# Performance work log

Hardware: AMD Instinct MI355X
Metric: run time of the kernel (lower is better)

Reference implementation:

```python
import math
import jax, jax.numpy as jnp
import numpy as np

C = 1024
H = 16
HD = C // H
T = 2048
B = 2
EPS = 1e-5


def setup_inputs() -> dict:
    key = jax.random.key(0)
    ks = jax.random.split(key, 8)
    s = 0.02
    return {
        "x": jax.random.normal(ks[0], (B, T, C), dtype=jnp.float32),
        "ln1_g": jnp.ones((C,), jnp.float32),
        "ln1_b": jnp.zeros((C,), jnp.float32),
        "w_attn": jax.random.normal(ks[1], (C, 3 * C), dtype=jnp.float32) * s,
        "b_attn": jnp.zeros((3 * C,), jnp.float32),
        "w_proj": jax.random.normal(ks[2], (C, C), dtype=jnp.float32) * s,
        "b_proj": jnp.zeros((C,), jnp.float32),
        "ln2_g": jnp.ones((C,), jnp.float32),
        "ln2_b": jnp.zeros((C,), jnp.float32),
        "w_fc": jax.random.normal(ks[3], (C, 4 * C), dtype=jnp.float32) * s,
        "b_fc": jnp.zeros((4 * C,), jnp.float32),
        "w_fc2": jax.random.normal(ks[4], (4 * C, C), dtype=jnp.float32) * s,
        "b_fc2": jnp.zeros((C,), jnp.float32),
    }


def _layernorm(x, g, b):
    mu = jnp.mean(x, axis=-1, keepdims=True)
    var = jnp.mean((x - mu) ** 2, axis=-1, keepdims=True)
    return (x - mu) * jax.lax.rsqrt(var + EPS) * g + b


def _attention(x, w_attn, b_attn, w_proj, b_proj):
    Bb, Tt, Cc = x.shape
    qkv = x @ w_attn + b_attn  # (B,T,3C)
    q, k, v = jnp.split(qkv, 3, axis=-1)
    # (B,H,T,HD)
    q = q.reshape(Bb, Tt, H, HD).transpose(0, 2, 1, 3)
    k = k.reshape(Bb, Tt, H, HD).transpose(0, 2, 1, 3)
    v = v.reshape(Bb, Tt, H, HD).transpose(0, 2, 1, 3)
    scale = 1.0 / math.sqrt(HD)
    attn = jnp.einsum("bhqd,bhkd->bhqk", q, k) * scale
    causal = jnp.tril(jnp.ones((Tt, Tt), dtype=bool))
    attn = jnp.where(causal[None, None], attn, -jnp.inf)
    attn = jax.nn.softmax(attn, axis=-1)
    out = jnp.einsum("bhqk,bhkd->bhqd", attn, v)
    out = out.transpose(0, 2, 1, 3).reshape(Bb, Tt, Cc)
    return out @ w_proj + b_proj


def _mlp(x, w_fc, b_fc, w_fc2, b_fc2):
    h = jax.nn.gelu(x @ w_fc + b_fc, approximate=True)
    return h @ w_fc2 + b_fc2


def reference(x, ln1_g, ln1_b, w_attn, b_attn, w_proj, b_proj,
              ln2_g, ln2_b, w_fc, b_fc, w_fc2, b_fc2):
    x = x + _attention(_layernorm(x, ln1_g, ln1_b), w_attn, b_attn, w_proj, b_proj)
    x = x + _mlp(_layernorm(x, ln2_g, ln2_b), w_fc, b_fc, w_fc2, b_fc2)
    return x
```

## Files before the change

### kernel.cpp

```cpp
#include <hip/hip_runtime.h>
#include <math.h>

#define TB 2
#define TT 2048
#define TC 1024
#define TH 16
#define THD 64
#define TM (TB*TT)
#define NQT 32

typedef __bf16 bf16x8 __attribute__((ext_vector_type(8)));
typedef float f32x4 __attribute__((ext_vector_type(4)));
typedef unsigned short u16x8 __attribute__((ext_vector_type(8)));
typedef unsigned short u16x4 __attribute__((ext_vector_type(4)));

__device__ __forceinline__ unsigned short f2bf(float f){
    unsigned int u = __builtin_bit_cast(unsigned int, f);
    u = (u + 0x7FFFu + ((u >> 16) & 1u)) >> 16;
    return (unsigned short)u;
}
__device__ __forceinline__ float bf2f(unsigned short h){
    unsigned int u = ((unsigned int)h) << 16;
    return __builtin_bit_cast(float, u);
}
__device__ __forceinline__ bf16x8 ldbf8(const unsigned short* p){
    return __builtin_bit_cast(bf16x8, *(const u16x8*)p);
}
__device__ __forceinline__ void gl_lds16(const void* g, void* l){
    __builtin_amdgcn_global_load_lds(
        (const __attribute__((address_space(1))) unsigned int*)g,
        (__attribute__((address_space(3))) unsigned int*)l,
        16, 0, 0);
}
__device__ __forceinline__ float gelu_tanh(float v){
    float u = 2.0f * 0.7978845608028654f * (v + 0.044715f * v * v * v);
    u = fminf(fmaxf(u, -30.f), 30.f);
    float e = __expf(u);
    return 0.5f * v * (1.f + (e - 1.f) / (e + 1.f));
}

__global__ __launch_bounds__(256)
void prep_all(const float* __restrict__ w_attn, const float* __restrict__ w_proj,
              const float* __restrict__ w_fc,   const float* __restrict__ w_fc2,
              unsigned short* __restrict__ wattnT, unsigned short* __restrict__ wprojT,
              unsigned short* __restrict__ wfcT,   unsigned short* __restrict__ wfc2T,
              const float* __restrict__ x, const float* __restrict__ ln1_g,
              const float* __restrict__ ln1_b, unsigned short* __restrict__ xn1){
    const int bid = blockIdx.x;
    const int t = threadIdx.x;
    if (bid >= 12288){
        const int row = bid - 12288;
        const float4* xr = (const float4*)(x + (size_t)row * TC);
        float4 v = xr[t];
        float s  = v.x + v.y + v.z + v.w;
        float s2 = v.x*v.x + v.y*v.y + v.z*v.z + v.w*v.w;
        #pragma unroll
        for (int off = 32; off; off >>= 1){
            s  += __shfl_down(s,  off);
            s2 += __shfl_down(s2, off);
        }
        __shared__ float red[8];
        int l = t & 63, wv = t >> 6;
        if (l == 0){ red[wv] = s; red[4 + wv] = s2; }
        __syncthreads();
        float S  = red[0] + red[1] + red[2] + red[3];
        float S2 = red[4] + red[5] + red[6] + red[7];
        float mu = S * (1.f / TC);
        float var = S2 * (1.f / TC) - mu * mu;
        float rs = rsqrtf(var + 1e-5f);
        int c = t * 4;
        float4 gg = *(const float4*)(ln1_g + c);
        float4 bb = *(const float4*)(ln1_b + c);
        u16x4 o;
        o[0] = f2bf((v.x - mu) * rs * gg.x + bb.x);
        o[1] = f2bf((v.y - mu) * rs * gg.y + bb.y);
        o[2] = f2bf((v.z - mu) * rs * gg.z + bb.z);
        o[3] = f2bf((v.w - mu) * rs * gg.w + bb.w);
        *(u16x4*)(xn1 + (size_t)row * TC + c) = o;
        return;
    }
    __shared__ float tile[32][33];
    const float* in; unsigned short* out; int K, N, bx, by;
    if (bid < 3072)      { in=w_attn; out=wattnT; K=1024; N=3072; bx=bid%96;  by=bid/96; }
    else if (bid < 4096) { int lo=bid-3072; in=w_proj; out=wprojT; K=1024; N=1024; bx=lo%32;  by=lo/32; }
    else if (bid < 8192) { int lo=bid-4096; in=w_fc;   out=wfcT;   K=1024; N=4096; bx=lo%128; by=lo/128; }
    else                 { int lo=bid-8192; in=w_fc2;  out=wfc2T;  K=4096; N=1024; bx=lo%32;  by=lo/32; }
    int tx = t & 31, ty = t >> 5;
    int n0 = bx * 32, k0 = by * 32;
    #pragma unroll
    for (int i = 0; i < 4; i++)
        tile[ty + 8*i][tx] = in[(size_t)(k0 + ty + 8*i) * N + n0 + tx];
    __syncthreads();
    #pragma unroll
    for (int i = 0; i < 4; i++)
        out[(size_t)(n0 + ty + 8*i) * K + k0 + tx] = f2bf(tile[tx][ty + 8*i]);
}

__global__ __launch_bounds__(256)
void ln_kernel(const float* __restrict__ x, const float* __restrict__ g,
               const float* __restrict__ be, unsigned short* __restrict__ y){
    const int row = blockIdx.x, t = threadIdx.x;
    const float4* xr = (const float4*)(x + (size_t)row * TC);
    float4 v = xr[t];
    float s  = v.x + v.y + v.z + v.w;
    float s2 = v.x*v.x + v.y*v.y + v.z*v.z + v.w*v.w;
    #pragma unroll
    for (int off = 32; off; off >>= 1){
        s  += __shfl_down(s,  off);
        s2 += __shfl_down(s2, off);
    }
    __shared__ float red[8];
    int l = t & 63, wv = t >> 6;
    if (l == 0){ red[wv] = s; red[4 + wv] = s2; }
    __syncthreads();
    float S  = red[0] + red[1] + red[2] + red[3];
    float S2 = red[4] + red[5] + red[6] + red[7];
    float mu = S * (1.f / TC);
    float var = S2 * (1.f / TC) - mu * mu;
    float rs = rsqrtf(var + 1e-5f);
    int c = t * 4;
    float4 gg = *(const float4*)(g + c);
    float4 bb = *(const float4*)(be + c);
    u16x4 o;
    o[0] = f2bf((v.x - mu) * rs * gg.x + bb.x);
    o[1] = f2bf((v.y - mu) * rs * gg.y + bb.y);
    o[2] = f2bf((v.z - mu) * rs * gg.z + bb.z);
    o[3] = f2bf((v.w - mu) * rs * gg.w + bb.w);
    *(u16x4*)(y + (size_t)row * TC + c) = o;
}

template<int EPI>
__global__ __launch_bounds__(256, 2)
void gemm_bt(const unsigned short* __restrict__ A,
             const unsigned short* __restrict__ Bt,
             const float* __restrict__ bias,
             const float* __restrict__ resid,
             void* __restrict__ outv,
             int M, int N, int K){
    __shared__ unsigned short lA[128 * 32];
    __shared__ unsigned short lB[128 * 32];
    const int t = threadIdx.x, w = t >> 6, l = t & 63, lr = l & 15, lg = l >> 4;
    const int nt = N >> 7;
    const int nwg = gridDim.x;
    const int bid = blockIdx.x;
    int wg = (nwg & 7) ? bid : ((bid & 7) * (nwg >> 3) + (bid >> 3));
    const int bm = wg / nt, bn = wg % nt;
    const int row0 = bm << 7, col0 = bn << 7;
    const int wr = w >> 1, wc = w & 1;

    f32x4 acc[4][4];
    #pragma unroll
    for (int i = 0; i < 4; i++)
        #pragma unroll
        for (int j = 0; j < 4; j++) acc[i][j] = (f32x4){0.f,0.f,0.f,0.f};

    const char* Ag = (const char*)(A + (size_t)(row0 + (t >> 2)) * K) + (t & 3) * 16;
    const char* Bg = (const char*)(Bt + (size_t)(col0 + (t >> 2)) * K) + (t & 3) * 16;
    const size_t rstep = (size_t)64 * K * 2;
    char* lAw = (char*)lA + w * 1024;
    char* lBw = (char*)lB + w * 1024;

    for (int k0 = 0; k0 < K; k0 += 32){
        size_t kb = (size_t)k0 * 2;
        gl_lds16(Ag + kb,          lAw);
        gl_lds16(Ag + kb + rstep,  lAw + 4096);
        gl_lds16(Bg + kb,          lBw);
        gl_lds16(Bg + kb + rstep,  lBw + 4096);
        __syncthreads();
        bf16x8 af[4], bfr[4];
        #pragma unroll
        for (int mi = 0; mi < 4; mi++)
            af[mi] = ldbf8(lA + (wr*64 + mi*16 + lr) * 32 + lg * 8);
        #pragma unroll
        for (int ni = 0; ni < 4; ni++)
            bfr[ni] = ldbf8(lB + (wc*64 + ni*16 + lr) * 32 + lg * 8);
        #pragma unroll
        for (int mi = 0; mi < 4; mi++)
            #pragma unroll
            for (int ni = 0; ni < 4; ni++)
                acc[mi][ni] = __builtin_amdgcn_mfma_f32_16x16x32_bf16(
                    af[mi], bfr[ni], acc[mi][ni], 0, 0, 0);
        __syncthreads();
    }

    float bcol[4];
    #pragma unroll
    for (int ni = 0; ni < 4; ni++) bcol[ni] = bias[col0 + wc*64 + ni*16 + lr];
    #pragma unroll
    for (int mi = 0; mi < 4; mi++){
        #pragma unroll
        for (int j = 0; j < 4; j++){
            int row = row0 + wr*64 + mi*16 + lg*4 + j;
            size_t base = (size_t)row * N + col0 + wc*64 + lr;
            #pragma unroll
            for (int ni = 0; ni < 4; ni++){
                float v = acc[mi][ni][j] + bcol[ni];
                size_t idx = base + (size_t)ni * 16;
                if (EPI == 0)      ((unsigned short*)outv)[idx] =
                    __builtin_bit_cast(unsigned short, (__bf16)v);
                else if (EPI == 1) ((float*)outv)[idx] = v + resid[idx];
                else               ((unsigned short*)outv)[idx] =
                    __builtin_bit_cast(unsigned short, (__bf16)gelu_tanh(v));
            }
        }
    }
}

template<int MH>
__device__ __forceinline__ void gloadA(const unsigned short* bufA, bf16x8 (&af)[4][2],
                                       int wm, int lr, int sl0, int sl1){
    #pragma unroll
    for (int i = 0; i < 4; i++){
        int lrow = (wm*128 + (MH*4 + i)*16 + lr) * 64;
        af[i][0] = ldbf8(bufA + lrow + sl0);
        af[i][1] = ldbf8(bufA + lrow + sl1);
    }
}
__device__ __forceinline__ void gloadB(const unsigned short* bufB, bf16x8 (&bfr)[4][2],
                                       int wn, int lr, int sl0, int sl1){
    #pragma unroll
    for (int i = 0; i < 4; i++){
        int brow = (wn*64 + i*16 + lr) * 64;
        bfr[i][0] = ldbf8(bufB + brow + sl0);
        bfr[i][1] = ldbf8(bufB + brow + sl1);
    }
}
template<int MH, int NH>
__device__ __forceinline__ void gmma(const bf16x8 (&af)[4][2], const bf16x8 (&bfr)[4][2],
                                     f32x4 (&acc)[8][4]){
    #pragma unroll
    for (int i = 0; i < 4; i++)
        #pragma unroll
        for (int j = 0; j < 2; j++){
            f32x4& a = acc[MH*4 + i][NH*2 + j];
            a = __builtin_amdgcn_mfma_f32_16x16x32_bf16(af[i][0], bfr[NH*2+j][0], a, 0,0,0);
            a = __builtin_amdgcn_mfma_f32_16x16x32_bf16(af[i][1], bfr[NH*2+j][1], a, 0,0,0);
        }
}

#define G256_LOOP(NT_, KBEG_)                                                   \
    for (int tk = 0; tk < (NT_); ++tk){                                         \
        const int cur = tk & 1;                                                 \
        const bool more1 = (tk + 1) < (NT_);                                    \
        const bool more2 = (tk + 2) < (NT_);                                    \
        const unsigned short* bufA = &lds[cur][0][0];                           \
        const unsigned short* bufB = &lds[cur][1][0];                           \
        if (more1) asm volatile("s_waitcnt vmcnt(2)" ::: "memory");             \
        else       asm volatile("s_waitcnt vmcnt(0)" ::: "memory");             \
        __builtin_amdgcn_s_barrier();                                           \
        {                                                                       \
            bf16x8 afr[4][2], bfr[4][2];                                        \
            gloadA<0>(bufA, afr, wm, lr, sl0, sl1);                             \
            gloadB(bufB, bfr, wn, lr, sl0, sl1);                                \
            if (more1){                                                         \
                stage(cur ^ 1, (KBEG_) + (tk + 1)*64, 1);                       \
                stage(cur ^ 1, (KBEG_) + (tk + 1)*64, 2);                       \
            }                                                                   \
            __builtin_amdgcn_s_setprio(1);                                      \
            gmma<0,0>(afr, bfr, acc);                                           \
            gmma<0,1>(afr, bfr, acc);                                           \
            __builtin_amdgcn_s_setprio(0);                                      \
            gloadA<1>(bufA, afr, wm, lr, sl0, sl1);                             \
            if (more1) stage(cur ^ 1, (KBEG_) + (tk + 1)*64, 3);                \
            __builtin_amdgcn_s_setprio(1);                                      \
            gmma<1,0>(afr, bfr, acc);                                           \
            gmma<1,1>(afr, bfr, acc);                                           \
            __builtin_amdgcn_s_setprio(0);                                      \
        }                                                                       \
        __builtin_amdgcn_s_barrier();                                           \
        if (more2) stage(cur, (KBEG_) + (tk + 2)*64, 0);                        \
    }

template<int EPI>
__global__ __launch_bounds__(512, 1)
void gemm256(const unsigned short* __restrict__ A,
             const unsigned short* __restrict__ Bt,
             const float* __restrict__ bias,
             void* __restrict__ outv,
             int M, int N, int K){
    __shared__ unsigned short lds[2][2][256*64];
    const int t = threadIdx.x;
    const int w = t >> 6, l = t & 63, lr = l & 15, lg = l >> 4;
    const int wm = w >> 2, wn = w & 3;
    const int lr7 = lr & 7;
    const int sl0 = (lg ^ lr7) << 3;
    const int sl1 = ((4 + lg) ^ lr7) << 3;
    const int nbn = N >> 8;
    const int nwg = (M >> 8) * nbn;
    const int bid = blockIdx.x;
    const int wg = (nwg & 7) ? bid : ((bid & 7) * (nwg >> 3) + (bid >> 3));
    const int bm = wg / nbn, bn = wg % nbn;
    const size_t row0 = (size_t)bm << 8, col0 = (size_t)bn << 8;
    const int NT = K >> 6;

    f32x4 acc[8][4];
    #pragma unroll
    for (int i = 0; i < 8; i++)
        #pragma unroll
        for (int j = 0; j < 4; j++) acc[i][j] = (f32x4){0.f,0.f,0.f,0.f};

    int rowc[4], slogc[4];
    #pragma unroll
    for (int c = 0; c < 4; c++){
        int seg = t + (c << 9);
        rowc[c]  = seg >> 3;
        slogc[c] = (((seg & 7) ^ ((seg >> 3) & 7)) << 3);
    }
    const unsigned short* Abase = A  + row0 * K;
    const unsigned short* Bbase = Bt + col0 * K;
    auto stage = [&](int buf, int kofs, int c){
        int seg = t + (c << 9);
        const unsigned short* sa = Abase + (size_t)rowc[c] * K + kofs + slogc[c];
        const unsigned short* sb = Bbase + (size_t)rowc[c] * K + kofs + slogc[c];
        gl_lds16(sa, (void*)&lds[buf][0][seg * 8]);
        gl_lds16(sb, (void*)&lds[buf][1][seg * 8]);
    };

    #pragma unroll
    for (int c = 0; c < 4; c++) stage(0, 0, c);
    if (NT > 1) stage(1, 64, 0);

    G256_LOOP(NT, 0)

    float bcol[4];
    #pragma unroll
    for (int ni = 0; ni < 4; ni++) bcol[ni] = bias[col0 + wn*64 + ni*16 + lr];
    unsigned short* outp = (unsigned short*)outv;
    #pragma unroll
    for (int mi = 0; mi < 8; mi++){
        #pragma unroll
        for (int j = 0; j < 4; j++){
            size_t row = row0 + wm*128 + mi*16 + lg*4 + j;
            size_t base = row * N + col0 + wn*64 + lr;
            #pragma unroll
            for (int ni = 0; ni < 4; ni++){
                float v = acc[mi][ni][j] + bcol[ni];
                size_t idx = base + (size_t)ni * 16;
                if (EPI == 0) outp[idx] = __builtin_bit_cast(unsigned short, (__bf16)v);
                else          outp[idx] = __builtin_bit_cast(unsigned short, (__bf16)gelu_tanh(v));
            }
        }
    }
}

__global__ __launch_bounds__(512, 1)
void gemm256sk(const unsigned short* __restrict__ A,
               const unsigned short* __restrict__ Bt,
               unsigned short* __restrict__ pout,
               int M, int N, int K, int klen){
    __shared__ unsigned short lds[2][2][256*64];
    const int t = threadIdx.x;
    const int w = t >> 6, l = t & 63, lr = l & 15, lg = l >> 4;
    const int wm = w >> 2, wn = w & 3;
    const int lr7 = lr & 7;
    const int sl0 = (lg ^ lr7) << 3;
    const int sl1 = ((4 + lg) ^ lr7) << 3;
    const int nbn = N >> 8;
    const int ntile = (M >> 8) * nbn;
    const int nwg = gridDim.x;
    const int bid = blockIdx.x;
    int wg = (nwg & 7) ? bid : ((bid & 7) * (nwg >> 3) + (bid >> 3));
    const int kh = wg / ntile;
    wg -= kh * ntile;
    const int bm = wg / nbn, bn = wg % nbn;
    const size_t row0 = (size_t)bm << 8, col0 = (size_t)bn << 8;
    const int NT = klen >> 6;
    const int kbeg = kh * klen;

    f32x4 acc[8][4];
    #pragma unroll
    for (int i = 0; i < 8; i++)
        #pragma unroll
        for (int j = 0; j < 4; j++) acc[i][j] = (f32x4){0.f,0.f,0.f,0.f};

    int rowc[4], slogc[4];
    #pragma unroll
    for (int c = 0; c < 4; c++){
        int seg = t + (c << 9);
        rowc[c]  = seg >> 3;
        slogc[c] = (((seg & 7) ^ ((seg >> 3) & 7)) << 3);
    }
    const unsigned short* Abase = A  + row0 * K;
    const unsigned short* Bbase = Bt + col0 * K;
    auto stage = [&](int buf, int kofs, int c){
        int seg = t + (c << 9);
        const unsigned short* sa = Abase + (size_t)rowc[c] * K + kofs + slogc[c];
        const unsigned short* sb = Bbase + (size_t)rowc[c] * K + kofs + slogc[c];
        gl_lds16(sa, (void*)&lds[buf][0][seg * 8]);
        gl_lds16(sb, (void*)&lds[buf][1][seg * 8]);
    };

    #pragma unroll
    for (int c = 0; c < 4; c++) stage(0, kbeg, c);
    if (NT > 1) stage(1, kbeg + 64, 0);

    G256_LOOP(NT, kbeg)

    unsigned short* outp = pout + (size_t)kh * M * N;
    #pragma unroll
    for (int mi = 0; mi < 8; mi++){
        #pragma unroll
        for (int j = 0; j < 4; j++){
            size_t row = row0 + wm*128 + mi*16 + lg*4 + j;
            size_t base = row * N + col0 + wn*64 + lr;
            #pragma unroll
            for (int ni = 0; ni < 4; ni++)
                outp[base + (size_t)ni * 16] =
                    __builtin_bit_cast(unsigned short, (__bf16)acc[mi][ni][j]);
        }
    }
}

__global__ __launch_bounds__(256)
void combine_k4(const unsigned short* __restrict__ p,
                const float* __restrict__ bias, const float* __restrict__ resid,
                float* __restrict__ out){
    const size_t PS = (size_t)TM * TC;
    const int total = TM * TC / 4;
    for (int i = blockIdx.x * 256 + threadIdx.x; i < total; i += gridDim.x * 256){
        int e = i * 4;
        u16x4 a0 = *(const u16x4*)(p + e);
        u16x4 a1 = *(const u16x4*)(p + PS + e);
        u16x4 a2 = *(const u16x4*)(p + 2*PS + e);
        u16x4 a3 = *(const u16x4*)(p + 3*PS + e);
        float4 r = *(const float4*)(resid + e);
        float4 bb = *(const float4*)(bias + (e & (TC - 1)));
        float4 o;
        o.x = bf2f(a0[0]) + bf2f(a1[0]) + bf2f(a2[0]) + bf2f(a3[0]) + r.x + bb.x;
        o.y = bf2f(a0[1]) + bf2f(a1[1]) + bf2f(a2[1]) + bf2f(a3[1]) + r.y + bb.y;
        o.z = bf2f(a0[2]) + bf2f(a1[2]) + bf2f(a2[2]) + bf2f(a3[2]) + r.z + bb.z;
        o.w = bf2f(a0[3]) + bf2f(a1[3]) + bf2f(a2[3]) + bf2f(a3[3]) + r.w + bb.w;
        *(float4*)(out + e) = o;
    }
}

__global__ __launch_bounds__(256)
void vtrans(const unsigned short* __restrict__ qkv, unsigned short* __restrict__ vTg){
    __shared__ unsigned short lt[64][68];
    int kt = blockIdx.x & (NQT - 1);
    int bh = blockIdx.x >> 5;
    int h = bh & (TH - 1), b = bh >> 4;
    int t = threadIdx.x;
    int r = t >> 2, c4 = t & 3;
    const unsigned short* src = qkv + (size_t)(b*TT + kt*64 + r) * (3*TC) + 2*TC + h*THD;
    u16x8 a0 = *(const u16x8*)(src + c4*8);
    u16x8 a1 = *(const u16x8*)(src + 32 + c4*8);
    #pragma unroll
    for (int j = 0; j < 8; j++){
        lt[r][c4*8 + j]      = a0[j];
        lt[r][32 + c4*8 + j] = a1[j];
    }
    __syncthreads();
    int d = t >> 2;
    unsigned short* dst = vTg + ((size_t)bh * NQT + kt) * (64*80) + (size_t)d * 80;
    u16x8 o0, o1;
    #pragma unroll
    for (int j = 0; j < 8; j++){
        o0[j] = lt[c4*8 + j][d];
        o1[j] = lt[32 + c4*8 + j][d];
    }
    *(u16x8*)(dst + c4*8)      = o0;
    *(u16x8*)(dst + 32 + c4*8) = o1;
}

__global__ __launch_bounds__(256, 3)
void attn_kernel(const unsigned short* __restrict__ qkv,
                 const unsigned short* __restrict__ vTg,
                 unsigned short* __restrict__ attn_out){
    __shared__ unsigned short kbuf[128*64];
    __shared__ unsigned short vbuf[128*64];
    __shared__ unsigned short pl[4][16*136];

    const int bid = blockIdx.x;
    const int qrank = bid >> 5;
    const int bh = bid & 31;
    const int h = bh & (TH - 1), b = bh >> 4;
    const int qb = 31 - qrank;
    const int q0 = qb << 6;
    const int t = threadIdx.x, w = t >> 6, l = t & 63, lr = l & 15, lg = l >> 4;
    const int lr7 = lr & 7;
    const int sl0 = (lg ^ lr7) << 3;
    const int sl1 = ((4 + lg) ^ lr7) << 3;
    const float SC = 0.18033688011112042f;

    const int NP = (qb >> 1) + 1;
    const int qrow_base = q0 + w*16;
    const int myq = qrow_base + lr;

    const unsigned short* kgp[4];
    const unsigned short* vgp[4];
    #pragma unroll
    for (int p = 0; p < 4; p++){
        int vt = p*256 + t;
        int r  = vt >> 3;
        int sc = ((vt & 7) ^ (r & 7)) * 8;
        kgp[p] = qkv + (size_t)(b*TT + r) * (3*TC) + TC + h*THD + sc;
        vgp[p] = vTg + (size_t)bh * (NQT*64*80)
               + (size_t)(r >> 6) * (64*80) + (size_t)(r & 63) * 80 + sc;
    }
    const size_t kstep2 = (size_t)128 * (3*TC);
    const size_t vstep2 = (size_t)2 * (64*80);

    auto stage_k = [&](int pi){
        #pragma unroll
        for (int p = 0; p < 4; p++)
            gl_lds16(kgp[p] + (size_t)pi*kstep2, (void*)&kbuf[(p*256 + t)*8]);
    };
    auto stage_v = [&](int pi){
        #pragma unroll
        for (int p = 0; p < 4; p++)
            gl_lds16(vgp[p] + (size_t)pi*vstep2, (void*)&vbuf[(p*256 + t)*8]);
    };

    const unsigned short* qr =
        qkv + (size_t)(b*TT + myq) * (3*TC) + h*THD;
    bf16x8 q0f = ldbf8(qr + lg*8), q1f = ldbf8(qr + 32 + lg*8);

    bf16x8 ones;
    #pragma unroll
    for (int i = 0; i < 8; i++) ones[i] = (__bf16)1.0f;

    f32x4 o[5];
    float m = -1e30f;
    #pragma unroll
    for (int i = 0; i < 5; i++) o[i] = (f32x4){0.f,0.f,0.f,0.f};

    unsigned short* plw = &pl[w][0];

    stage_k(0);
    for (int pi = 0; pi < NP; ++pi){
        const int t0 = 2*pi, t1 = 2*pi + 1;
        asm volatile("s_waitcnt vmcnt(0)" ::: "memory");
        __builtin_amdgcn_s_barrier();
        stage_v(pi);

        f32x4 s[8];
        __builtin_amdgcn_s_setprio(1);
        #pragma unroll
        for (int cb = 0; cb < 8; cb++){
            bf16x8 ka = ldbf8(kbuf + (cb*16 + lr)*64 + sl0);
            bf16x8 kbf = ldbf8(kbuf + (cb*16 + lr)*64 + sl1);
            f32x4 z = (f32x4){0.f,0.f,0.f,0.f};
            z = __builtin_amdgcn_mfma_f32_16x16x32_bf16(ka, q0f, z, 0,0,0);
            z = __builtin_amdgcn_mfma_f32_16x16x32_bf16(kbf, q1f, z, 0,0,0);
            s[cb] = z;
        }
        __builtin_amdgcn_s_setprio(0);
        if (t0 == qb){
            #pragma unroll
            for (int cb = 0; cb < 4; cb++)
                #pragma unroll
                for (int j = 0; j < 4; j++)
                    if (t0*64 + cb*16 + lg*4 + j > myq) s[cb][j] = -1e30f;
        }
        if (t1 == qb){
            #pragma unroll
            for (int cb = 4; cb < 8; cb++)
                #pragma unroll
                for (int j = 0; j < 4; j++)
                    if (t1*64 + (cb-4)*16 + lg*4 + j > myq) s[cb][j] = -1e30f;
        } else if (t1 > qb){
            #pragma unroll
            for (int cb = 4; cb < 8; cb++)
                #pragma unroll
                for (int j = 0; j < 4; j++) s[cb][j] = -1e30f;
        }
        float mloc = s[0][0];
        #pragma unroll
        for (int cb = 0; cb < 8; cb++)
            #pragma unroll
            for (int j = 0; j < 4; j++) mloc = fmaxf(mloc, s[cb][j]);
        mloc = fmaxf(mloc, __shfl_xor(mloc, 16));
        mloc = fmaxf(mloc, __shfl_xor(mloc, 32));
        bool grow = (mloc * SC > m);
        float al = 1.f;
        if (__any(grow)){
            float mn = fmaxf(m, mloc * SC);
            al = exp2f(m - mn);
            m = mn;
            float alb[4];
            #pragma unroll
            for (int j = 0; j < 4; j++) alb[j] = __shfl(al, lg*4 + j);
            #pragma unroll
            for (int db = 0; db < 5; db++)
                #pragma unroll
                for (int j = 0; j < 4; j++) o[db][j] *= alb[j];
        }
        #pragma unroll
        for (int cb = 0; cb < 8; cb++){
            u16x4 pk;
            #pragma unroll
            for (int j = 0; j < 4; j++){
                float e = exp2f(__builtin_fmaf(s[cb][j], SC, -m));
                pk[j] = __builtin_bit_cast(unsigned short, (__bf16)e);
            }
            *(u16x4*)(plw + lr*136 + cb*16 + lg*4) = pk;
        }
        asm volatile("s_waitcnt vmcnt(0)" ::: "memory");
        __builtin_amdgcn_s_barrier();
        if (pi + 1 < NP) stage_k(pi + 1);

        bf16x8 pa0 = ldbf8(plw + lr*136 + lg*8);
        bf16x8 pa1 = ldbf8(plw + lr*136 + 32 + lg*8);
        bf16x8 pa2 = ldbf8(plw + lr*136 + 64 + lg*8);
        bf16x8 pa3 = ldbf8(plw + lr*136 + 96 + lg*8);
        __builtin_amdgcn_s_setprio(1);
        #pragma unroll
        for (int db = 0; db < 4; db++){
            bf16x8 v0a = ldbf8(vbuf + (db*16 + lr)*64 + sl0);
            bf16x8 v0b = ldbf8(vbuf + (db*16 + lr)*64 + sl1);
            o[db] = __builtin_amdgcn_mfma_f32_16x16x32_bf16(pa0, v0a, o[db], 0,0,0);
            o[db] = __builtin_amdgcn_mfma_f32_16x16x32_bf16(pa1, v0b, o[db], 0,0,0);
            bf16x8 v1a = ldbf8(vbuf + (64 + db*16 + lr)*64 + sl0);
            bf16x8 v1b = ldbf8(vbuf + (64 + db*16 + lr)*64 + sl1);
            o[db] = __builtin_amdgcn_mfma_f32_16x16x32_bf16(pa2, v1a, o[db], 0,0,0);
            o[db] = __builtin_amdgcn_mfma_f32_16x16x32_bf16(pa3, v1b, o[db], 0,0,0);
        }
        o[4] = __builtin_amdgcn_mfma_f32_16x16x32_bf16(pa0, ones, o[4], 0,0,0);
        o[4] = __builtin_amdgcn_mfma_f32_16x16x32_bf16(pa1, ones, o[4], 0,0,0);
        o[4] = __builtin_amdgcn_mfma_f32_16x16x32_bf16(pa2, ones, o[4], 0,0,0);
        o[4] = __builtin_amdgcn_mfma_f32_16x16x32_bf16(pa3, ones, o[4], 0,0,0);
        __builtin_amdgcn_s_setprio(0);
    }

    __bf16* aout = (__bf16*)attn_out;
    #pragma unroll
    for (int j = 0; j < 4; j++){
        float inv = 1.f / o[4][j];
        size_t tok = (size_t)(b*TT + qrow_base + lg*4 + j);
        #pragma unroll
        for (int db = 0; db < 4; db++)
            aout[tok*TC + h*THD + db*16 + lr] = (__bf16)(o[db][j] * inv);
    }
}

extern "C" void kernel_launch(void* const* d_in, const int* in_sizes, int n_in,
                              void* d_out, int out_size, void* d_ws, size_t ws_size,
                              hipStream_t stream){
    const float* x      = (const float*)d_in[0];
    const float* ln1_g  = (const float*)d_in[1];
    const float* ln1_b  = (const float*)d_in[2];
    const float* w_attn = (const float*)d_in[3];
    const float* b_attn = (const float*)d_in[4];
    const float* w_proj = (const float*)d_in[5];
    const float* b_proj = (const float*)d_in[6];
    const float* ln2_g  = (const float*)d_in[7];
    const float* ln2_b  = (const float*)d_in[8];
    const float* w_fc   = (const float*)d_in[9];
    const float* b_fc   = (const float*)d_in[10];
    const float* w_fc2  = (const float*)d_in[11];
    const float* b_fc2  = (const float*)d_in[12];
    float* out = (float*)d_out;

    char* ws = (char*)d_ws;
    size_t off = 0;
    auto alloc = [&](size_t bytes) -> void* {
        void* p = ws + off;
        off += (bytes + 255) & ~(size_t)255;
        return p;
    };
    unsigned short* wattnT = (unsigned short*)alloc((size_t)3072*1024*2);
    unsigned short* wprojT = (unsigned short*)alloc((size_t)1024*1024*2);
    unsigned short* wfcT   = (unsigned short*)alloc((size_t)4096*1024*2);
    unsigned short* wfc2T  = (unsigned short*)alloc((size_t)1024*4096*2);
    unsigned short* xn1    = (unsigned short*)alloc((size_t)TM*TC*2);
    unsigned short* qkvb   = (unsigned short*)alloc((size_t)TM*3*TC*2);
    float*          resid1 = (float*)alloc((size_t)TM*TC*4);
    unsigned short* xn2    = (unsigned short*)alloc((size_t)TM*TC*2);
    unsigned short* hbuf   = (unsigned short*)alloc((size_t)TM*4*TC*2);
    unsigned short* attnO  = (unsigned short*)alloc((size_t)TM*TC*2);
    unsigned short* vTg    = (unsigned short*)alloc((size_t)TB*TH*NQT*64*80*2);

    unsigned short* pks = xn1;

    prep_all<<<12288 + TM, 256, 0, stream>>>(
        w_attn, w_proj, w_fc, w_fc2, wattnT, wprojT, wfcT, wfc2T,
        x, ln1_g, ln1_b, xn1);

    gemm256<0><<<(TM/256)*(3072/256), 512, 0, stream>>>(
        xn1, wattnT, b_attn, qkvb, TM, 3072, 1024);

    vtrans<<<TB*TH*NQT, 256, 0, stream>>>(qkvb, vTg);

    attn_kernel<<<TB*TH*NQT, 256, 0, stream>>>(qkvb, vTg, attnO);

    gemm_bt<1><<<(TM/128)*(1024/128), 256, 0, stream>>>(
        attnO, wprojT, b_proj, x, resid1, TM, 1024, 1024);

    ln_kernel<<<TM, 256, 0, stream>>>(resid1, ln2_g, ln2_b, xn2);

    gemm256<2><<<(TM/256)*(4096/256), 512, 0, stream>>>(
        xn2, wfcT, b_fc, hbuf, TM, 4096, 1024);

    gemm256sk<<<4*(TM/256)*(1024/256), 512, 0, stream>>>(
        hbuf, wfc2T, pks, TM, 1024, 4096, 1024);
    combine_k4<<<2048, 256, 0, stream>>>(pks, b_fc2, resid1, out);
}
```

Baseline: 211.7 us.

## Restructure 256-tile GEMM into triple-buffered K32 pipeline and skip masked attention blocks

The 256x256 GEMM kernels are merged into one template that covers the split-K case. Its main loop now uses 32-wide K slices with three LDS buffers, issues the next-but-one stage before waiting, and runs a full 8x4 MFMA block per step with no XOR swizzle on the LDS layout. Separately, the attention kernel skips the QK, softmax and PV work for the second 64-key half of a pair whenever that half lies entirely past the causal diagonal, instead of computing it and masking it to -inf. The unswizzled LDS layout may cause bank conflicts, and the smaller K step doubles the number of barriers per tile.

```diff
diff --git a/kernel.cpp b/kernel.cpp
--- a/kernel.cpp
+++ b/kernel.cpp
@@ -206,165 +206,27 @@
     }
 }
 
-template<int MH>
-__device__ __forceinline__ void gloadA(const unsigned short* bufA, bf16x8 (&af)[4][2],
-                                       int wm, int lr, int sl0, int sl1){
-    #pragma unroll
-    for (int i = 0; i < 4; i++){
-        int lrow = (wm*128 + (MH*4 + i)*16 + lr) * 64;
-        af[i][0] = ldbf8(bufA + lrow + sl0);
-        af[i][1] = ldbf8(bufA + lrow + sl1);
-    }
-}
-__device__ __forceinline__ void gloadB(const unsigned short* bufB, bf16x8 (&bfr)[4][2],
-                                       int wn, int lr, int sl0, int sl1){
-    #pragma unroll
-    for (int i = 0; i < 4; i++){
-        int brow = (wn*64 + i*16 + lr) * 64;
-        bfr[i][0] = ldbf8(bufB + brow + sl0);
-        bfr[i][1] = ldbf8(bufB + brow + sl1);
-    }
-}
-template<int MH, int NH>
-__device__ __forceinline__ void gmma(const bf16x8 (&af)[4][2], const bf16x8 (&bfr)[4][2],
-                                     f32x4 (&acc)[8][4]){
-    #pragma unroll
-    for (int i = 0; i < 4; i++)
-        #pragma unroll
-        for (int j = 0; j < 2; j++){
-            f32x4& a = acc[MH*4 + i][NH*2 + j];
-            a = __builtin_amdgcn_mfma_f32_16x16x32_bf16(af[i][0], bfr[NH*2+j][0], a, 0,0,0);
-            a = __builtin_amdgcn_mfma_f32_16x16x32_bf16(af[i][1], bfr[NH*2+j][1], a, 0,0,0);
-        }
-}
-
-#define G256_LOOP(NT_, KBEG_)                                                   \
-    for (int tk = 0; tk < (NT_); ++tk){                                         \
-        const int cur = tk & 1;                                                 \
-        const bool more1 = (tk + 1) < (NT_);                                    \
-        const bool more2 = (tk + 2) < (NT_);                                    \
-        const unsigned short* bufA = &lds[cur][0][0];                           \
-        const unsigned short* bufB = &lds[cur][1][0];                           \
-        if (more1) asm volatile("s_waitcnt vmcnt(2)" ::: "memory");             \
-        else       asm volatile("s_waitcnt vmcnt(0)" ::: "memory");             \
-        __builtin_amdgcn_s_barrier();                                           \
-        {                                                                       \
-            bf16x8 afr[4][2], bfr[4][2];                                        \
-            gloadA<0>(bufA, afr, wm, lr, sl0, sl1);                             \
-            gloadB(bufB, bfr, wn, lr, sl0, sl1);                                \
-            if (more1){                                                         \
-                stage(cur ^ 1, (KBEG_) + (tk + 1)*64, 1);                       \
-                stage(cur ^ 1, (KBEG_) + (tk + 1)*64, 2);                       \
-            }                                                                   \
-            __builtin_amdgcn_s_setprio(1);                                      \
-            gmma<0,0>(afr, bfr, acc);                                           \
-            gmma<0,1>(afr, bfr, acc);                                           \
-            __builtin_amdgcn_s_setprio(0);                                      \
-            gloadA<1>(bufA, afr, wm, lr, sl0, sl1);                             \
-            if (more1) stage(cur ^ 1, (KBEG_) + (tk + 1)*64, 3);                \
-            __builtin_amdgcn_s_setprio(1);                                      \
-            gmma<1,0>(afr, bfr, acc);                                           \
-            gmma<1,1>(afr, bfr, acc);                                           \
-            __builtin_amdgcn_s_setprio(0);                                      \
-        }                                                                       \
-        __builtin_amdgcn_s_barrier();                                           \
-        if (more2) stage(cur, (KBEG_) + (tk + 2)*64, 0);                        \
-    }
-
 template<int EPI>
 __global__ __launch_bounds__(512, 1)
 void gemm256(const unsigned short* __restrict__ A,
              const unsigned short* __restrict__ Bt,
              const float* __restrict__ bias,
              void* __restrict__ outv,
-             int M, int N, int K){
-    __shared__ unsigned short lds[2][2][256*64];
+             int M, int N, int K, int klen){
+    __shared__ unsigned short lds[3][2][256*32];
     const int t = threadIdx.x;
     const int w = t >> 6, l = t & 63, lr = l & 15, lg = l >> 4;
     const int wm = w >> 2, wn = w & 3;
-    const int lr7 = lr & 7;
-    const int sl0 = (lg ^ lr7) << 3;
-    const int sl1 = ((4 + lg) ^ lr7) << 3;
-    const int nbn = N >> 8;
-    const int nwg = (M >> 8) * nbn;
-    const int bid = blockIdx.x;
-    const int wg = (nwg & 7) ? bid : ((bid & 7) * (nwg >> 3) + (bid >> 3));
-    const int bm = wg / nbn, bn = wg % nbn;
-    const size_t row0 = (size_t)bm << 8, col0 = (size_t)bn << 8;
-    const int NT = K >> 6;
-
-    f32x4 acc[8][4];
-    #pragma unroll
-    for (int i = 0; i < 8; i++)
-        #pragma unroll
-        for (int j = 0; j < 4; j++) acc[i][j] = (f32x4){0.f,0.f,0.f,0.f};
-
-    int rowc[4], slogc[4];
-    #pragma unroll
-    for (int c = 0; c < 4; c++){
-        int seg = t + (c << 9);
-        rowc[c]  = seg >> 3;
-        slogc[c] = (((seg & 7) ^ ((seg >> 3) & 7)) << 3);
-    }
-    const unsigned short* Abase = A  + row0 * K;
-    const unsigned short* Bbase = Bt + col0 * K;
-    auto stage = [&](int buf, int kofs, int c){
-        int seg = t + (c << 9);
-        const unsigned short* sa = Abase + (size_t)rowc[c] * K + kofs + slogc[c];
-        const unsigned short* sb = Bbase + (size_t)rowc[c] * K + kofs + slogc[c];
-        gl_lds16(sa, (void*)&lds[buf][0][seg * 8]);
-        gl_lds16(sb, (void*)&lds[buf][1][seg * 8]);
-    };
-
-    #pragma unroll
-    for (int c = 0; c < 4; c++) stage(0, 0, c);
-    if (NT > 1) stage(1, 64, 0);
-
-    G256_LOOP(NT, 0)
-
-    float bcol[4];
-    #pragma unroll
-    for (int ni = 0; ni < 4; ni++) bcol[ni] = bias[col0 + wn*64 + ni*16 + lr];
-    unsigned short* outp = (unsigned short*)outv;
-    #pragma unroll
-    for (int mi = 0; mi < 8; mi++){
-        #pragma unroll
-        for (int j = 0; j < 4; j++){
-            size_t row = row0 + wm*128 + mi*16 + lg*4 + j;
-            size_t base = row * N + col0 + wn*64 + lr;
-            #pragma unroll
-            for (int ni = 0; ni < 4; ni++){
-                float v = acc[mi][ni][j] + bcol[ni];
-                size_t idx = base + (size_t)ni * 16;
-                if (EPI == 0) outp[idx] = __builtin_bit_cast(unsigned short, (__bf16)v);
-                else          outp[idx] = __builtin_bit_cast(unsigned short, (__bf16)gelu_tanh(v));
-            }
-        }
-    }
-}
-
-__global__ __launch_bounds__(512, 1)
-void gemm256sk(const unsigned short* __restrict__ A,
-               const unsigned short* __restrict__ Bt,
-               unsigned short* __restrict__ pout,
-               int M, int N, int K, int klen){
-    __shared__ unsigned short lds[2][2][256*64];
-    const int t = threadIdx.x;
-    const int w = t >> 6, l = t & 63, lr = l & 15, lg = l >> 4;
-    const int wm = w >> 2, wn = w & 3;
-    const int lr7 = lr & 7;
-    const int sl0 = (lg ^ lr7) << 3;
-    const int sl1 = ((4 + lg) ^ lr7) << 3;
     const int nbn = N >> 8;
     const int ntile = (M >> 8) * nbn;
     const int nwg = gridDim.x;
     const int bid = blockIdx.x;
     int wg = (nwg & 7) ? bid : ((bid & 7) * (nwg >> 3) + (bid >> 3));
-    const int kh = wg / ntile;
+    const int kh = (EPI == 3) ? (wg / ntile) : 0;
     wg -= kh * ntile;
     const int bm = wg / nbn, bn = wg % nbn;
     const size_t row0 = (size_t)bm << 8, col0 = (size_t)bn << 8;
-    const int NT = klen >> 6;
+    const int NT = klen >> 5;
     const int kbeg = kh * klen;
 
     f32x4 acc[8][4];
@@ -373,30 +235,59 @@
         #pragma unroll
         for (int j = 0; j < 4; j++) acc[i][j] = (f32x4){0.f,0.f,0.f,0.f};
 
-    int rowc[4], slogc[4];
-    #pragma unroll
-    for (int c = 0; c < 4; c++){
-        int seg = t + (c << 9);
-        rowc[c]  = seg >> 3;
-        slogc[c] = (((seg & 7) ^ ((seg >> 3) & 7)) << 3);
-    }
     const unsigned short* Abase = A  + row0 * K;
     const unsigned short* Bbase = Bt + col0 * K;
-    auto stage = [&](int buf, int kofs, int c){
-        int seg = t + (c << 9);
-        const unsigned short* sa = Abase + (size_t)rowc[c] * K + kofs + slogc[c];
-        const unsigned short* sb = Bbase + (size_t)rowc[c] * K + kofs + slogc[c];
-        gl_lds16(sa, (void*)&lds[buf][0][seg * 8]);
-        gl_lds16(sb, (void*)&lds[buf][1][seg * 8]);
+    const int r0 = t >> 2,          ks0 = (t & 3) * 8;
+    const int r1 = (512 + t) >> 2,  ks1 = ks0;
+    auto stage = [&](int buf, int kofs){
+        gl_lds16(Abase + (size_t)r0 * K + kofs + ks0, (void*)&lds[buf][0][t*8]);
+        gl_lds16(Bbase + (size_t)r0 * K + kofs + ks0, (void*)&lds[buf][1][t*8]);
+        gl_lds16(Abase + (size_t)r1 * K + kofs + ks1, (void*)&lds[buf][0][(512 + t)*8]);
+        gl_lds16(Bbase + (size_t)r1 * K + kofs + ks1, (void*)&lds[buf][1][(512 + t)*8]);
     };
 
-    #pragma unroll
-    for (int c = 0; c < 4; c++) stage(0, kbeg, c);
-    if (NT > 1) stage(1, kbeg + 64, 0);
-
-    G256_LOOP(NT, kbeg)
-
-    unsigned short* outp = pout + (size_t)kh * M * N;
+    stage(0, kbeg);
+    stage(1, kbeg + 32);
+
+    for (int tk = 0; tk < NT; ++tk){
+        const int cur = tk % 3;
+        const bool more2 = (tk + 2) < NT;
+        const bool more1 = (tk + 1) < NT;
+        if (more2) stage((tk + 2) % 3, kbeg + (tk + 2) * 32);
+        if (more2)      asm volatile("s_waitcnt vmcnt(8)" ::: "memory");
+        else if (more1) asm volatile("s_waitcnt vmcnt(4)" ::: "memory");
+        else            asm volatile("s_waitcnt vmcnt(0)" ::: "memory");
+        __builtin_amdgcn_s_barrier();
+
+        bf16x8 afr[8], bfr[4];
+        #pragma unroll
+        for (int mb = 0; mb < 8; mb++)
+            afr[mb] = ldbf8(&lds[cur][0][(wm*128 + mb*16 + lr)*32 + lg*8]);
+        #pragma unroll
+        for (int nb = 0; nb < 4; nb++)
+            bfr[nb] = ldbf8(&lds[cur][1][(wn*64 + nb*16 + lr)*32 + lg*8]);
+        asm volatile("s_waitcnt lgkmcnt(0)" ::: "memory");
+        __builtin_amdgcn_sched_barrier(0);
+        __builtin_amdgcn_s_setprio(1);
+        #pragma unroll
+        for (int mb = 0; mb < 8; mb++)
+            #pragma unroll
+            for (int nb = 0; nb < 4; nb++)
+                acc[mb][nb] = __builtin_amdgcn_mfma_f32_16x16x32_bf16(
+                    afr[mb], bfr[nb], acc[mb][nb], 0, 0, 0);
+        __builtin_amdgcn_s_setprio(0);
+        __builtin_amdgcn_s_barrier();
+    }
+
+    unsigned short* outp;
+    float bcol[4];
+    if (EPI == 3){
+        outp = (unsigned short*)outv + (size_t)kh * M * N;
+    } else {
+        outp = (unsigned short*)outv;
+        #pragma unroll
+        for (int ni = 0; ni < 4; ni++) bcol[ni] = bias[col0 + wn*64 + ni*16 + lr];
+    }
     #pragma unroll
     for (int mi = 0; mi < 8; mi++){
         #pragma unroll
@@ -404,9 +295,16 @@
             size_t row = row0 + wm*128 + mi*16 + lg*4 + j;
             size_t base = row * N + col0 + wn*64 + lr;
             #pragma unroll
-            for (int ni = 0; ni < 4; ni++)
-                outp[base + (size_t)ni * 16] =
-                    __builtin_bit_cast(unsigned short, (__bf16)acc[mi][ni][j]);
+            for (int ni = 0; ni < 4; ni++){
+                size_t idx = base + (size_t)ni * 16;
+                if (EPI == 3)
+                    outp[idx] = __builtin_bit_cast(unsigned short, (__bf16)acc[mi][ni][j]);
+                else {
+                    float v = acc[mi][ni][j] + bcol[ni];
+                    if (EPI == 0) outp[idx] = __builtin_bit_cast(unsigned short, (__bf16)v);
+                    else          outp[idx] = __builtin_bit_cast(unsigned short, (__bf16)gelu_tanh(v));
+                }
+            }
         }
     }
 }
@@ -530,6 +428,7 @@
     stage_k(0);
     for (int pi = 0; pi < NP; ++pi){
         const int t0 = 2*pi, t1 = 2*pi + 1;
+        const bool full = (t1 <= qb);
         asm volatile("s_waitcnt vmcnt(0)" ::: "memory");
         __builtin_amdgcn_s_barrier();
         stage_v(pi);
@@ -537,7 +436,7 @@
         f32x4 s[8];
         __builtin_amdgcn_s_setprio(1);
         #pragma unroll
-        for (int cb = 0; cb < 8; cb++){
+        for (int cb = 0; cb < 4; cb++){
             bf16x8 ka = ldbf8(kbuf + (cb*16 + lr)*64 + sl0);
             bf16x8 kbf = ldbf8(kbuf + (cb*16 + lr)*64 + sl1);
             f32x4 z = (f32x4){0.f,0.f,0.f,0.f};
@@ -545,6 +444,17 @@
             z = __builtin_amdgcn_mfma_f32_16x16x32_bf16(kbf, q1f, z, 0,0,0);
             s[cb] = z;
         }
+        if (full){
+            #pragma unroll
+            for (int cb = 4; cb < 8; cb++){
+                bf16x8 ka = ldbf8(kbuf + (cb*16 + lr)*64 + sl0);
+                bf16x8 kbf = ldbf8(kbuf + (cb*16 + lr)*64 + sl1);
+                f32x4 z = (f32x4){0.f,0.f,0.f,0.f};
+                z = __builtin_amdgcn_mfma_f32_16x16x32_bf16(ka, q0f, z, 0,0,0);
+                z = __builtin_amdgcn_mfma_f32_16x16x32_bf16(kbf, q1f, z, 0,0,0);
+                s[cb] = z;
+            }
+        }
         __builtin_amdgcn_s_setprio(0);
         if (t0 == qb){
             #pragma unroll
@@ -553,30 +463,30 @@
                 for (int j = 0; j < 4; j++)
                     if (t0*64 + cb*16 + lg*4 + j > myq) s[cb][j] = -1e30f;
         }
-        if (t1 == qb){
+        if (full && t1 == qb){
             #pragma unroll
             for (int cb = 4; cb < 8; cb++)
                 #pragma unroll
                 for (int j = 0; j < 4; j++)
                     if (t1*64 + (cb-4)*16 + lg*4 + j > myq) s[cb][j] = -1e30f;
-        } else if (t1 > qb){
+        }
+        float mloc = s[0][0];
+        #pragma unroll
+        for (int cb = 0; cb < 4; cb++)
+            #pragma unroll
+            for (int j = 0; j < 4; j++) mloc = fmaxf(mloc, s[cb][j]);
+        if (full){
             #pragma unroll
             for (int cb = 4; cb < 8; cb++)
                 #pragma unroll
-                for (int j = 0; j < 4; j++) s[cb][j] = -1e30f;
-        }
-        float mloc = s[0][0];
-        #pragma unroll
-        for (int cb = 0; cb < 8; cb++)
-            #pragma unroll
-            for (int j = 0; j < 4; j++) mloc = fmaxf(mloc, s[cb][j]);
+                for (int j = 0; j < 4; j++) mloc = fmaxf(mloc, s[cb][j]);
+        }
         mloc = fmaxf(mloc, __shfl_xor(mloc, 16));
         mloc = fmaxf(mloc, __shfl_xor(mloc, 32));
         bool grow = (mloc * SC > m);
-        float al = 1.f;
         if (__any(grow)){
             float mn = fmaxf(m, mloc * SC);
-            al = exp2f(m - mn);
+            float al = exp2f(m - mn);
             m = mn;
             float alb[4];
             #pragma unroll
@@ -587,7 +497,7 @@
                 for (int j = 0; j < 4; j++) o[db][j] *= alb[j];
         }
         #pragma unroll
-        for (int cb = 0; cb < 8; cb++){
+        for (int cb = 0; cb < 4; cb++){
             u16x4 pk;
             #pragma unroll
             for (int j = 0; j < 4; j++){
@@ -596,14 +506,24 @@
             }
             *(u16x4*)(plw + lr*136 + cb*16 + lg*4) = pk;
         }
+        if (full){
+            #pragma unroll
+            for (int cb = 4; cb < 8; cb++){
+                u16x4 pk;
+                #pragma unroll
+                for (int j = 0; j < 4; j++){
+                    float e = exp2f(__builtin_fmaf(s[cb][j], SC, -m));
+                    pk[j] = __builtin_bit_cast(unsigned short, (__bf16)e);
+                }
+                *(u16x4*)(plw + lr*136 + cb*16 + lg*4) = pk;
+            }
+        }
         asm volatile("s_waitcnt vmcnt(0)" ::: "memory");
         __builtin_amdgcn_s_barrier();
         if (pi + 1 < NP) stage_k(pi + 1);
 
         bf16x8 pa0 = ldbf8(plw + lr*136 + lg*8);
         bf16x8 pa1 = ldbf8(plw + lr*136 + 32 + lg*8);
-        bf16x8 pa2 = ldbf8(plw + lr*136 + 64 + lg*8);
-        bf16x8 pa3 = ldbf8(plw + lr*136 + 96 + lg*8);
         __builtin_amdgcn_s_setprio(1);
         #pragma unroll
         for (int db = 0; db < 4; db++){
@@ -611,15 +531,22 @@
             bf16x8 v0b = ldbf8(vbuf + (db*16 + lr)*64 + sl1);
             o[db] = __builtin_amdgcn_mfma_f32_16x16x32_bf16(pa0, v0a, o[db], 0,0,0);
             o[db] = __builtin_amdgcn_mfma_f32_16x16x32_bf16(pa1, v0b, o[db], 0,0,0);
-            bf16x8 v1a = ldbf8(vbuf + (64 + db*16 + lr)*64 + sl0);
-            bf16x8 v1b = ldbf8(vbuf + (64 + db*16 + lr)*64 + sl1);
-            o[db] = __builtin_amdgcn_mfma_f32_16x16x32_bf16(pa2, v1a, o[db], 0,0,0);
-            o[db] = __builtin_amdgcn_mfma_f32_16x16x32_bf16(pa3, v1b, o[db], 0,0,0);
         }
         o[4] = __builtin_amdgcn_mfma_f32_16x16x32_bf16(pa0, ones, o[4], 0,0,0);
         o[4] = __builtin_amdgcn_mfma_f32_16x16x32_bf16(pa1, ones, o[4], 0,0,0);
-        o[4] = __builtin_amdgcn_mfma_f32_16x16x32_bf16(pa2, ones, o[4], 0,0,0);
-        o[4] = __builtin_amdgcn_mfma_f32_16x16x32_bf16(pa3, ones, o[4], 0,0,0);
+        if (full){
+            bf16x8 pa2 = ldbf8(plw + lr*136 + 64 + lg*8);
+            bf16x8 pa3 = ldbf8(plw + lr*136 + 96 + lg*8);
+            #pragma unroll
+            for (int db = 0; db < 4; db++){
+                bf16x8 v1a = ldbf8(vbuf + (64 + db*16 + lr)*64 + sl0);
+                bf16x8 v1b = ldbf8(vbuf + (64 + db*16 + lr)*64 + sl1);
+                o[db] = __builtin_amdgcn_mfma_f32_16x16x32_bf16(pa2, v1a, o[db], 0,0,0);
+                o[db] = __builtin_amdgcn_mfma_f32_16x16x32_bf16(pa3, v1b, o[db], 0,0,0);
+            }
+            o[4] = __builtin_amdgcn_mfma_f32_16x16x32_bf16(pa2, ones, o[4], 0,0,0);
+            o[4] = __builtin_amdgcn_mfma_f32_16x16x32_bf16(pa3, ones, o[4], 0,0,0);
+        }
         __builtin_amdgcn_s_setprio(0);
     }
 
@@ -678,7 +605,7 @@
         x, ln1_g, ln1_b, xn1);
 
     gemm256<0><<<(TM/256)*(3072/256), 512, 0, stream>>>(
-        xn1, wattnT, b_attn, qkvb, TM, 3072, 1024);
+        xn1, wattnT, b_attn, qkvb, TM, 3072, 1024, 1024);
 
     vtrans<<<TB*TH*NQT, 256, 0, stream>>>(qkvb, vTg);
 
@@ -690,9 +617,9 @@
     ln_kernel<<<TM, 256, 0, stream>>>(resid1, ln2_g, ln2_b, xn2);
 
     gemm256<2><<<(TM/256)*(4096/256), 512, 0, stream>>>(
-        xn2, wfcT, b_fc, hbuf, TM, 4096, 1024);
-
-    gemm256sk<<<4*(TM/256)*(1024/256), 512, 0, stream>>>(
-        hbuf, wfc2T, pks, TM, 1024, 4096, 1024);
+        xn2, wfcT, b_fc, hbuf, TM, 4096, 1024, 1024);
+
+    gemm256<3><<<4*(TM/256)*(1024/256), 512, 0, stream>>>(
+        hbuf, wfc2T, nullptr, pks, TM, 1024, 4096, 1024);
     combine_k4<<<2048, 256, 0, stream>>>(pks, b_fc2, resid1, out);
 }
```

Result: slower. 230.7 us (+9.0%).
